# Kernel optimization log

Hardware: AMD Instinct MI355X
Metric: run time of the kernel (lower is better)

Reference implementation:

```python
import jax, jax.numpy as jnp
import numpy as np

D_MODEL = 1024
NUM_HEADS = 16
D_K = D_MODEL // NUM_HEADS
B, S = 4, 2048
NEG = -1e20


def setup_inputs() -> dict:
    key = jax.random.key(0)
    ks = jax.random.split(key, 12)
    def lin(kw, kb):
        # torch nn.Linear init: U(-1/sqrt(in), 1/sqrt(in)), weight shape [out, in]
        bound = 1.0 / np.sqrt(D_MODEL)
        W = jax.random.uniform(kw, (D_MODEL, D_MODEL), jnp.float32, -bound, bound)
        b = jax.random.uniform(kb, (D_MODEL,), jnp.float32, -bound, bound)
        return W, b
    Wq, bq = lin(ks[0], ks[1])
    Wk, bk = lin(ks[2], ks[3])
    Wv, bv = lin(ks[4], ks[5])
    Wo, bo = lin(ks[6], ks[7])
    q = jax.random.normal(ks[8], (B, S, D_MODEL), jnp.float32)
    k = jax.random.normal(ks[9], (B, S, D_MODEL), jnp.float32)
    v = jax.random.normal(ks[10], (B, S, D_MODEL), jnp.float32)
    # causal mask, broadcastable [1,1,S,S]; mask==0 positions are masked out
    mask = jnp.tril(jnp.ones((S, S), jnp.int32))[None, None]
    return {"q": q, "k": k, "v": v, "mask": mask,
            "Wq": Wq, "bq": bq, "Wk": Wk, "bk": bk,
            "Wv": Wv, "bv": bv, "Wo": Wo, "bo": bo}


def _split_heads(x):
    b, s, _ = x.shape
    return x.reshape(b, s, NUM_HEADS, D_K).transpose(0, 2, 1, 3)  # [b,h,s,dk]


def reference(q, k, v, mask, Wq, bq, Wk, bk, Wv, bv, Wo, bo):
    qh = _split_heads(q @ Wq.T + bq)
    kh = _split_heads(k @ Wk.T + bk)
    vh = _split_heads(v @ Wv.T + bv)
    scores = jnp.einsum('bhqd,bhkd->bhqk', qh, kh) / jnp.sqrt(jnp.float32(D_K))
    scores = jnp.where(mask == 0, jnp.float32(NEG), scores)
    attn = jax.nn.softmax(scores, axis=-1)  # dropout is identity in eval mode
    out = jnp.einsum('bhqk,bhkd->bhqd', attn, vh)
    out = out.transpose(0, 2, 1, 3).reshape(q.shape[0], -1, D_MODEL)
    return out @ Wo.T + bo, attn
```

## Files before the change

kernel.cpp:

```cpp
#include <hip/hip_runtime.h>
#include <stdint.h>

#define S_LEN 2048
#define NHEADS 16
#define DK 64
#define DMODEL 1024
#define PS_STRIDE 72
#define S_MASK -3.0e4f

typedef __bf16 bf16;
typedef __bf16 bf16x8 __attribute__((ext_vector_type(8)));
typedef float f32x4 __attribute__((ext_vector_type(4)));
typedef uint32_t u32;

#define MFMA(a, b, c) __builtin_amdgcn_mfma_f32_16x16x32_bf16((a), (b), (c), 0, 0, 0)

#define WAVE_LGKM0()                                       \
  do {                                                     \
    asm volatile("s_waitcnt lgkmcnt(0)" ::: "memory");     \
    __builtin_amdgcn_sched_barrier(0);                     \
  } while (0)
#define BAR_VM16()                                         \
  do {                                                     \
    asm volatile("s_waitcnt vmcnt(16)" ::: "memory");      \
    __builtin_amdgcn_sched_barrier(0);                     \
    __builtin_amdgcn_s_barrier();                          \
    __builtin_amdgcn_sched_barrier(0);                     \
  } while (0)

__device__ __forceinline__ bf16x8 cvt8(f32x4 a, f32x4 b) {
  bf16x8 w;
  w[0] = (bf16)a[0]; w[1] = (bf16)a[1]; w[2] = (bf16)a[2]; w[3] = (bf16)a[3];
  w[4] = (bf16)b[0]; w[5] = (bf16)b[1]; w[6] = (bf16)b[2]; w[7] = (bf16)b[3];
  return w;
}

__device__ __forceinline__ void async16(const void* g, void* lds_uniform) {
  __builtin_amdgcn_global_load_lds((const __attribute__((address_space(1))) u32*)g,
                                   (__attribute__((address_space(3))) u32*)lds_uniform,
                                   16, 0, 0);
}

__device__ __forceinline__ void stage_tile8(const bf16* gbase, size_t rstride,
                                            bf16* buf, int wave, int lane) {
  int c = wave * 64 + lane;
  int r = c >> 3, ch = c & 7;
  int chg = ch ^ (r & 7);
  const bf16* src = gbase + (size_t)r * rstride + chg * 8;
  char* dst = (char*)buf + (size_t)(wave * 64) * 16;
  async16(src, dst);
}

__global__ __launch_bounds__(256) void cvt_f32_bf16(const float* __restrict__ src,
                                                    bf16* __restrict__ dst, int n8) {
  int stride = gridDim.x * blockDim.x;
  for (int i = blockIdx.x * blockDim.x + threadIdx.x; i < n8; i += stride) {
    f32x4 a = ((const f32x4*)src)[2 * i];
    f32x4 b = ((const f32x4*)src)[2 * i + 1];
    ((bf16x8*)dst)[i] = cvt8(a, b);
  }
}

template <int MODE, typename OutT>
__global__ __launch_bounds__(256, 2) void gemm_bias(const bf16* __restrict__ X,
                                                    const bf16* __restrict__ W,
                                                    const float* __restrict__ bias,
                                                    OutT* __restrict__ out) {
  __shared__ __attribute__((aligned(16))) bf16 At[128 * 32];
  __shared__ __attribute__((aligned(16))) bf16 Bt[128 * 32];
  const int tid = threadIdx.x;
  const int wave = tid >> 6;
  const int lane = tid & 63;
  const int col16 = lane & 15;
  const int kg = lane >> 4;
  const int m0 = blockIdx.x * 128;
  const int n0 = blockIdx.y * 128;
  const int wm = (wave >> 1) * 64;
  const int wn = (wave & 1) * 64;

  f32x4 acc[4][4] = {};

  for (int k0 = 0; k0 < 1024; k0 += 32) {
    __syncthreads();
#pragma unroll
    for (int is = 0; is < 2; ++is) {
      int idx = wave * 64 + is * 256 + lane;
      int row = idx >> 2, ch = idx & 3;
      const char* ga = (const char*)(X + (size_t)(m0 + row) * 1024 + k0) + ch * 16;
      const char* gb = (const char*)(W + (size_t)(n0 + row) * 1024 + k0) + ch * 16;
      async16(ga, (char*)At + (size_t)(wave * 64 + is * 256) * 16);
      async16(gb, (char*)Bt + (size_t)(wave * 64 + is * 256) * 16);
    }
    __syncthreads();

    bf16x8 af[4], bfr[4];
#pragma unroll
    for (int i = 0; i < 4; ++i)
      af[i] = *(const bf16x8*)&At[(wm + i * 16 + col16) * 32 + kg * 8];
#pragma unroll
    for (int j = 0; j < 4; ++j)
      bfr[j] = *(const bf16x8*)&Bt[(wn + j * 16 + col16) * 32 + kg * 8];
#pragma unroll
    for (int i = 0; i < 4; ++i)
#pragma unroll
      for (int j = 0; j < 4; ++j) acc[i][j] = MFMA(af[i], bfr[j], acc[i][j]);
  }

#pragma unroll
  for (int j = 0; j < 4; ++j) {
    int n = n0 + wn + j * 16 + col16;
    float bj = bias[n];
#pragma unroll
    for (int i = 0; i < 4; ++i) {
#pragma unroll
      for (int r = 0; r < 4; ++r) {
        int m = m0 + wm + i * 16 + kg * 4 + r;
        float v = acc[i][j][r] + bj;
        size_t o;
        if (MODE == 0) {
          o = (size_t)m * 1024 + n;
        } else {
          int b = m >> 11, s = m & 2047;
          int h = n >> 6, d = n & 63;
          if (MODE == 1)
            o = ((size_t)(b * 16 + h) * 2048 + s) * 64 + d;
          else
            o = ((size_t)(b * 16 + h) * 64 + d) * 2048 + s;
        }
        out[o] = (OutT)v;
      }
    }
  }
}

__global__ __launch_bounds__(512, 4) void attn_fused(const bf16* __restrict__ Qh,
                                                     const bf16* __restrict__ Kh,
                                                     const bf16* __restrict__ Vt,
                                                     float* __restrict__ attn,
                                                     bf16* __restrict__ O) {
  __shared__ __attribute__((aligned(16))) bf16 Klds[2][64 * 64];
  __shared__ __attribute__((aligned(16))) bf16 Vlds[2][64 * 64];
  __shared__ __attribute__((aligned(16))) bf16 Ps[128 * PS_STRIDE];
  const int tid = threadIdx.x;
  const int wave = tid >> 6;
  const int lane = tid & 63;
  const int col16 = lane & 15;
  const int kg = lane >> 4;
  const int pr = blockIdx.x;
  const int bh = blockIdx.z * NHEADS + blockIdx.y;

  const bf16* qb = Qh + (size_t)bh * S_LEN * DK;
  const bf16* kb = Kh + (size_t)bh * S_LEN * DK;
  const bf16* vb = Vt + (size_t)bh * DK * S_LEN;
  float* ab = attn + (size_t)bh * S_LEN * S_LEN;
  const int b_ = bh >> 4, h_ = bh & 15;

#pragma unroll 1
  for (int sp = 0; sp < 2; ++sp) {
    const int bq = sp ? (15 - pr) : pr;
    const int q0 = bq * 128;
    const int jt_max = 2 * bq + 1;

    bf16x8 qf[2];
#pragma unroll
    for (int kk = 0; kk < 2; ++kk) {
      bf16x8 v = *(const bf16x8*)&qb[(size_t)(q0 + wave * 16 + col16) * DK + kk * 32 + kg * 8];
      bf16x8 sc;
#pragma unroll
      for (int e = 0; e < 8; ++e) sc[e] = (bf16)((float)v[e] * 0.125f);
      qf[kk] = sc;
    }

    float l_run[4] = {};

    stage_tile8(kb, DK, Klds[0], wave, lane);
    __syncthreads();
    int cur = 0;
    for (int jt = 0; jt <= jt_max; ++jt) {
      if (jt < jt_max) stage_tile8(kb + (size_t)(jt + 1) * 64 * DK, DK, Klds[cur ^ 1], wave, lane);
      const int j0 = jt * 64;
      f32x4 s[4] = {};
#pragma unroll
      for (int kk = 0; kk < 2; ++kk) {
        bf16x8 kf[4];
#pragma unroll
        for (int fc = 0; fc < 4; ++fc) {
          int rr = fc * 16 + col16;
          kf[fc] = *(const bf16x8*)&Klds[cur][rr * 64 + (((kk << 2) + kg) ^ (rr & 7)) * 8];
        }
#pragma unroll
        for (int fc = 0; fc < 4; ++fc) s[fc] = MFMA(qf[kk], kf[fc], s[fc]);
      }
      if (jt >= 2 * bq) {
#pragma unroll
        for (int fc = 0; fc < 4; ++fc)
#pragma unroll
          for (int r = 0; r < 4; ++r) {
            int qi = q0 + wave * 16 + kg * 4 + r;
            int j = j0 + fc * 16 + col16;
            if (j > qi) s[fc][r] = S_MASK;
          }
      }
#pragma unroll
      for (int r = 0; r < 4; ++r)
        l_run[r] += (__expf(s[0][r]) + __expf(s[1][r])) + (__expf(s[2][r]) + __expf(s[3][r]));
      __syncthreads();
      cur ^= 1;
    }
    float linv[4];
#pragma unroll
    for (int r = 0; r < 4; ++r) {
      float l = l_run[r];
#pragma unroll
      for (int dd = 1; dd < 16; dd <<= 1) l += __shfl_xor(l, dd, 64);
      linv[r] = 1.f / l;
    }

    {
      f32x4 z = {0.f, 0.f, 0.f, 0.f};
      for (int jt = jt_max + 1; jt < S_LEN / 64; ++jt) {
        const int j0 = jt * 64;
#pragma unroll
        for (int rep = 0; rep < 4; ++rep) {
          int idx = rep * 512 + tid;
          int row = idx >> 4, c = idx & 15;
          *(f32x4*)&ab[(size_t)(q0 + row) * S_LEN + j0 + c * 4] = z;
        }
      }
    }

    f32x4 o[4] = {};
    stage_tile8(kb, DK, Klds[0], wave, lane);
    stage_tile8(vb, S_LEN, Vlds[0], wave, lane);
    __syncthreads();
    cur = 0;
    for (int jt = 0; jt <= jt_max; ++jt) {
      if (jt < jt_max) {
        stage_tile8(kb + (size_t)(jt + 1) * 64 * DK, DK, Klds[cur ^ 1], wave, lane);
        stage_tile8(vb + (jt + 1) * 64, S_LEN, Vlds[cur ^ 1], wave, lane);
      }
      const int j0 = jt * 64;
      f32x4 s[4] = {};
#pragma unroll
      for (int kk = 0; kk < 2; ++kk) {
        bf16x8 kf[4];
#pragma unroll
        for (int fc = 0; fc < 4; ++fc) {
          int rr = fc * 16 + col16;
          kf[fc] = *(const bf16x8*)&Klds[cur][rr * 64 + (((kk << 2) + kg) ^ (rr & 7)) * 8];
        }
#pragma unroll
        for (int fc = 0; fc < 4; ++fc) s[fc] = MFMA(qf[kk], kf[fc], s[fc]);
      }
      if (jt >= 2 * bq) {
#pragma unroll
        for (int fc = 0; fc < 4; ++fc)
#pragma unroll
          for (int r = 0; r < 4; ++r) {
            int qi = q0 + wave * 16 + kg * 4 + r;
            int j = j0 + fc * 16 + col16;
            if (j > qi) s[fc][r] = S_MASK;
          }
      }
#pragma unroll
      for (int fc = 0; fc < 4; ++fc)
#pragma unroll
        for (int r = 0; r < 4; ++r) {
          float p = __expf(s[fc][r]) * linv[r];
          int row = wave * 16 + kg * 4 + r;
          int col = fc * 16 + col16;
          ab[(size_t)(q0 + row) * S_LEN + j0 + col] = p;
          Ps[row * PS_STRIDE + col] = (bf16)p;
        }
      WAVE_LGKM0();
#pragma unroll
      for (int kk = 0; kk < 2; ++kk) {
        bf16x8 pf, vf[4];
        pf = *(const bf16x8*)&Ps[(wave * 16 + col16) * PS_STRIDE + kk * 32 + kg * 8];
#pragma unroll
        for (int fc = 0; fc < 4; ++fc) {
          int rr = fc * 16 + col16;
          vf[fc] = *(const bf16x8*)&Vlds[cur][rr * 64 + (((kk << 2) + kg) ^ (rr & 7)) * 8];
        }
#pragma unroll
        for (int fc = 0; fc < 4; ++fc) o[fc] = MFMA(pf, vf[fc], o[fc]);
      }
      BAR_VM16();
      cur ^= 1;
    }

#pragma unroll
    for (int fc = 0; fc < 4; ++fc)
#pragma unroll
      for (int r = 0; r < 4; ++r) {
        size_t row = (size_t)b_ * S_LEN + q0 + wave * 16 + kg * 4 + r;
        O[row * DMODEL + h_ * 64 + fc * 16 + col16] = (bf16)o[fc][r];
      }
    __syncthreads();
  }
}

static inline void cvt_launch(const float* src, bf16* dst, size_t n, hipStream_t stream) {
  int n8 = (int)(n / 8);
  int blocks = (n8 + 255) / 256;
  if (blocks > 2048) blocks = 2048;
  cvt_f32_bf16<<<blocks, 256, 0, stream>>>(src, dst, n8);
}

extern "C" void kernel_launch(void* const* d_in, const int* in_sizes, int n_in,
                              void* d_out, int out_size, void* d_ws, size_t ws_size,
                              hipStream_t stream) {
  (void)in_sizes; (void)n_in; (void)out_size; (void)ws_size;
  const float* q = (const float*)d_in[0];
  const float* k = (const float*)d_in[1];
  const float* v = (const float*)d_in[2];
  const float* Wq = (const float*)d_in[4];
  const float* bq = (const float*)d_in[5];
  const float* Wk = (const float*)d_in[6];
  const float* bk = (const float*)d_in[7];
  const float* Wv = (const float*)d_in[8];
  const float* bv = (const float*)d_in[9];
  const float* Wo = (const float*)d_in[10];
  const float* bo = (const float*)d_in[11];

  float* out = (float*)d_out;
  float* attn = out + (size_t)8192 * 1024;

  const size_t NX = (size_t)8192 * 1024;
  const size_t NW = (size_t)1024 * 1024;
  bf16* Qh = (bf16*)d_ws;
  bf16* Kh = Qh + NX;
  bf16* Vt = Kh + NX;
  bf16* O = Vt + NX;
  bf16* Xbf = O + NX;
  bf16* Wbf = Xbf + NX;

  dim3 gg(64, 8), bb(256);

  cvt_launch(q, Xbf, NX, stream);
  cvt_launch(Wq, Wbf, NW, stream);
  gemm_bias<1, bf16><<<gg, bb, 0, stream>>>(Xbf, Wbf, bq, Qh);

  cvt_launch(k, Xbf, NX, stream);
  cvt_launch(Wk, Wbf, NW, stream);
  gemm_bias<1, bf16><<<gg, bb, 0, stream>>>(Xbf, Wbf, bk, Kh);

  cvt_launch(v, Xbf, NX, stream);
  cvt_launch(Wv, Wbf, NW, stream);
  gemm_bias<2, bf16><<<gg, bb, 0, stream>>>(Xbf, Wbf, bv, Vt);

  attn_fused<<<dim3(8, NHEADS, 4), 512, 0, stream>>>(Qh, Kh, Vt, attn, O);

  cvt_launch(Wo, Wbf, NW, stream);
  gemm_bias<0, float><<<gg, bb, 0, stream>>>(O, Wbf, bo, out);
}
```

Measured before the change: 480.3 us.

## Interleave attention zero-fill stores into the row-sum pass loop

```diff
diff --git a/kernel.cpp b/kernel.cpp
--- a/kernel.cpp
+++ b/kernel.cpp
@@ -18,6 +18,13 @@
 #define WAVE_LGKM0()                                       \
   do {                                                     \
     asm volatile("s_waitcnt lgkmcnt(0)" ::: "memory");     \
+    __builtin_amdgcn_sched_barrier(0);                     \
+  } while (0)
+#define BAR_VM4()                                          \
+  do {                                                     \
+    asm volatile("s_waitcnt vmcnt(4)" ::: "memory");       \
+    __builtin_amdgcn_sched_barrier(0);                     \
+    __builtin_amdgcn_s_barrier();                          \
     __builtin_amdgcn_sched_barrier(0);                     \
   } while (0)
 #define BAR_VM16()                                         \
@@ -49,6 +56,17 @@
   const bf16* src = gbase + (size_t)r * rstride + chg * 8;
   char* dst = (char*)buf + (size_t)(wave * 64) * 16;
   async16(src, dst);
+}
+
+__device__ __forceinline__ void zero_tile(float* __restrict__ ab, int q0z,
+                                          int j0z, int tid) {
+  f32x4 z = {0.f, 0.f, 0.f, 0.f};
+#pragma unroll
+  for (int rep = 0; rep < 4; ++rep) {
+    int idx = rep * 512 + tid;
+    int row = idx >> 4, c = idx & 15;
+    *(f32x4*)&ab[(size_t)(q0z + row) * S_LEN + j0z + c * 4] = z;
+  }
 }
 
 __global__ __launch_bounds__(256) void cvt_f32_bf16(const float* __restrict__ src,
@@ -155,9 +173,12 @@
   float* ab = attn + (size_t)bh * S_LEN * S_LEN;
   const int b_ = bh >> 4, h_ = bh & 15;
 
+  int zq = 0;
+  const int zq_heavy = 2 * pr;
+
 #pragma unroll 1
   for (int sp = 0; sp < 2; ++sp) {
-    const int bq = sp ? (15 - pr) : pr;
+    const int bq = sp ? pr : (15 - pr);
     const int q0 = bq * 128;
     const int jt_max = 2 * bq + 1;
 
@@ -204,7 +225,19 @@
 #pragma unroll
       for (int r = 0; r < 4; ++r)
         l_run[r] += (__expf(s[0][r]) + __expf(s[1][r])) + (__expf(s[2][r]) + __expf(s[3][r]));
-      __syncthreads();
+      if (zq < 30) {
+        int q0z, jtz;
+        if (zq < zq_heavy) {
+          q0z = (15 - pr) * 128;
+          jtz = 2 * (15 - pr) + 2 + zq;
+        } else {
+          q0z = pr * 128;
+          jtz = 2 * pr + 2 + (zq - zq_heavy);
+        }
+        zero_tile(ab, q0z, jtz * 64, tid);
+        ++zq;
+      }
+      BAR_VM4();
       cur ^= 1;
     }
     float linv[4];
@@ -214,19 +247,6 @@
 #pragma unroll
       for (int dd = 1; dd < 16; dd <<= 1) l += __shfl_xor(l, dd, 64);
       linv[r] = 1.f / l;
-    }
-
-    {
-      f32x4 z = {0.f, 0.f, 0.f, 0.f};
-      for (int jt = jt_max + 1; jt < S_LEN / 64; ++jt) {
-        const int j0 = jt * 64;
-#pragma unroll
-        for (int rep = 0; rep < 4; ++rep) {
-          int idx = rep * 512 + tid;
-          int row = idx >> 4, c = idx & 15;
-          *(f32x4*)&ab[(size_t)(q0 + row) * S_LEN + j0 + c * 4] = z;
-        }
-      }
     }
 
     f32x4 o[4] = {};
```

Result: slower. 506.6 us (+5.5%).
